# Kernel tuning notes

Hardware: AMD Instinct MI355X
Metric: run time of the kernel (lower is better)

Reference implementation:

```python
import jax, jax.numpy as jnp
import numpy as np
from jax.ops import segment_sum, segment_max

N_NODES, SEQ, D, V = 2048, 64, 256, 32000
NH, DH = 8, 32      # transformer heads, head dim
GH = 4              # GAT heads (concat=False -> mean over heads)
E = 32768
NEG_INF = -1e9


def _pe(max_len, d):
    pos = np.arange(max_len)[:, None].astype(np.float32)
    div = np.exp(np.arange(0, d, 2).astype(np.float32) * (-np.log(10000.0) / d))
    pe = np.zeros((max_len, d), np.float32)
    pe[:, 0::2] = np.sin(pos * div)
    pe[:, 1::2] = np.cos(pos * div)
    return jnp.asarray(pe)


def _ln(x, g, b, eps=1e-5):
    m = x.mean(-1, keepdims=True)
    v = jnp.var(x, axis=-1, keepdims=True)
    return (x - m) / jnp.sqrt(v + eps) * g + b


def _encoder(x, Wqkv, bqkv, Wo, bo, ln1g, ln1b, ln2g, ln2b, W1, b1, W2, b2):
    # nn.TransformerEncoder, post-norm, relu, dropout off (eval)
    for l in range(2):
        qkv = x @ Wqkv[l] + bqkv[l]
        q, k, v = jnp.split(qkv, 3, -1)
        hds = lambda t: t.reshape(N_NODES, SEQ, NH, DH).transpose(0, 2, 1, 3)
        q, k, v = hds(q), hds(k), hds(v)
        att = jax.nn.softmax(jnp.einsum('bhqd,bhkd->bhqk', q, k) / np.sqrt(DH).astype(np.float32), -1)
        o = jnp.einsum('bhqk,bhkd->bhqd', att, v).transpose(0, 2, 1, 3).reshape(N_NODES, SEQ, D)
        x = _ln(x + o @ Wo[l] + bo[l], ln1g[l], ln1b[l])
        ff = jax.nn.relu(x @ W1[l] + b1[l]) @ W2[l] + b2[l]
        x = _ln(x + ff, ln2g[l], ln2b[l])
    return x


def _gat(xt, W, b, asrc, adst, src, dst, emask):
    # PyG GATConv(heads=4, concat=False): self-loops added, LeakyReLU(0.2),
    # softmax over incoming edges per destination, mean over heads, + bias.
    x = (xt @ W).reshape(N_NODES, GH, D)              # [N,GH,D]
    a_s = jnp.sum(x * asrc, -1)                        # [N,GH]
    a_d = jnp.sum(x * adst, -1)
    e = jax.nn.leaky_relu(a_s[src] + a_d[dst], 0.2)    # [E,GH]
    e = jnp.where(emask[:, None], e, NEG_INF)
    e_self = jax.nn.leaky_relu(a_s + a_d, 0.2)         # [N,GH] self loops
    m = jnp.maximum(segment_max(e, dst, num_segments=N_NODES), e_self)
    w = jnp.where(emask[:, None], jnp.exp(e - m[dst]), 0.0)
    w_self = jnp.exp(e_self - m)
    denom = segment_sum(w, dst, num_segments=N_NODES) + w_self
    num = segment_sum(w[:, :, None] * x[src], dst, num_segments=N_NODES) + w_self[:, :, None] * x
    return (num / denom[:, :, None]).mean(1) + b


def setup_inputs():
    key = jax.random.key(0)
    ks = iter(jax.random.split(key, 40))
    g = lambda shape, s=0.02: jax.random.normal(next(ks), shape, jnp.float32) * s
    return dict(
        tok_emb=g((V, D)),
        enc_Wqkv=g((2, D, 3 * D)), enc_bqkv=jnp.zeros((2, 3 * D)),
        enc_Wo=g((2, D, D)), enc_bo=jnp.zeros((2, D)),
        enc_ln1_g=jnp.ones((2, D)), enc_ln1_b=jnp.zeros((2, D)),
        enc_ln2_g=jnp.ones((2, D)), enc_ln2_b=jnp.zeros((2, D)),
        enc_W1=g((2, D, D)), enc_b1=jnp.zeros((2, D)),
        enc_W2=g((2, D, D)), enc_b2=jnp.zeros((2, D)),
        type_emb=g((10, D)),
        msg_W=g((3, D, D)), msg_b=jnp.zeros((3, D)),
        gat_W=g((4, D, GH * D)), gat_b=jnp.zeros((4, D)),
        gat_asrc=g((4, GH, D)), gat_adst=g((4, GH, D)),
        sp_W1=g((D, 512)), sp_b1=jnp.zeros((512,)),
        sp_W2=g((512, D)), sp_b2=jnp.zeros((D,)),
        log_c=jnp.zeros((1,)),
        rule_token_seqs=jax.random.randint(next(ks), (N_NODES, SEQ), 0, V),
        rule_types=jax.random.randint(next(ks), (N_NODES,), 0, 10),
        edge_index=jax.random.randint(next(ks), (2, E), 0, N_NODES),
        edge_type=jax.random.randint(next(ks), (E,), 0, 3),
    )


def reference(tok_emb, enc_Wqkv, enc_bqkv, enc_Wo, enc_bo, enc_ln1_g, enc_ln1_b,
              enc_ln2_g, enc_ln2_b, enc_W1, enc_b1, enc_W2, enc_b2, type_emb,
              msg_W, msg_b, gat_W, gat_b, gat_asrc, gat_adst,
              sp_W1, sp_b1, sp_W2, sp_b2, log_c,
              rule_token_seqs, rule_types, edge_index, edge_type):
    # logic encoder
    x = tok_emb[rule_token_seqs] * np.sqrt(D).astype(np.float32) + _pe(SEQ, D)[None]
    x = _encoder(x, enc_Wqkv, enc_bqkv, enc_Wo, enc_bo, enc_ln1_g, enc_ln1_b,
                 enc_ln2_g, enc_ln2_b, enc_W1, enc_b1, enc_W2, enc_b2)
    h = x.mean(1) + type_emb[rule_types]                 # node_features [N,D]
    # logical GNN: per-relation linear + GATConv, summed, residual, relu
    src, dst = edge_index[0], edge_index[1]
    for l in range(4):
        h_new = 0.0
        for r in range(3):
            th = h @ msg_W[r] + msg_b[r]
            h_new = h_new + _gat(th, gat_W[l], gat_b[l], gat_asrc[l], gat_adst[l],
                                 src, dst, edge_type == r)
        h = jax.nn.relu(h + h_new)
    pos = jax.nn.relu(h @ sp_W1 + sp_b1) @ sp_W2 + sp_b2
    tang = jnp.tanh(pos) * 2.0
    st = tang * jnp.sqrt(jnp.exp(log_c))                 # scaled tangent [N,D]
    # Lorentz exp_map0 of v = [0, st]: ||v||_L = ||st||
    r = jnp.maximum(jnp.linalg.norm(st, axis=-1, keepdims=True), 1e-8)
    return jnp.concatenate([jnp.cosh(r), jnp.sinh(r) / r * st], -1)  # [N, D+1]
```

## Files before the change

kernel.cpp:

```cpp
#include <hip/hip_runtime.h>
#include <hip/hip_bf16.h>

#define NN 2048
#define SEQL 64
#define DIM 256
#define NHEAD 8
#define EDGES 32768
#define CHUNKS 2
#define CN (NN / CHUNKS)
#define CROWS (CN * SEQL)

typedef __attribute__((ext_vector_type(8))) short short8;
typedef __attribute__((ext_vector_type(4))) float f32x4;
typedef __attribute__((ext_vector_type(4))) unsigned short us4;
typedef unsigned short ushort_t;

__device__ __forceinline__ float us2f(unsigned short u) {
    union { unsigned int i; float f; } x; x.i = ((unsigned int)u) << 16; return x.f;
}
__device__ __forceinline__ unsigned short f2us(float f) {
    union { float f; unsigned int i; } u; u.f = f;
    unsigned int r = u.i + 0x7fffu + ((u.i >> 16) & 1u);
    return (unsigned short)(r >> 16);
}
__device__ __forceinline__ float lrelu02(float v) { return v < 0.f ? 0.2f * v : v; }

__device__ __forceinline__ void gload_lds16(const void* g, void* l) {
    __builtin_amdgcn_global_load_lds(
        (const __attribute__((address_space(1))) unsigned int*)g,
        (__attribute__((address_space(3))) unsigned int*)l, 16, 0, 0);
}

__global__ void sniff_kernel(const unsigned int* __restrict__ w, int* __restrict__ flag) {
    __shared__ int cnt;
    if (threadIdx.x == 0) cnt = 0;
    __syncthreads();
    unsigned int v = w[(size_t)threadIdx.x * 509];
    unsigned int e_lo = (v >> 7) & 0xffu;
    if (e_lo >= 0x6eu && e_lo <= 0x7fu) atomicAdd(&cnt, 1);
    __syncthreads();
    if (threadIdx.x == 0) *flag = (cnt > 128) ? 1 : 0;
}

#define NE 33
struct ConvArgs {
    const void* src[NE];
    unsigned int soff[NE];
    unsigned int off[NE + 1];
    unsigned int nel[NE];
    unsigned short ncol[NE];
    unsigned char klog2[NE];
};

__global__ void convert_kernel(ConvArgs a, const int* __restrict__ flag,
                               ushort_t* __restrict__ dst, unsigned int total) {
    const int bf = *flag;
    for (unsigned int i = blockIdx.x * 256 + threadIdx.x; i < total; i += gridDim.x * 256) {
        int e = 0;
        while (a.off[e + 1] <= i) ++e;
        unsigned int j = i - a.off[e];
        ushort_t v = 0;
        if (j < a.nel[e]) {
            unsigned int sidx;
            if (a.klog2[e]) {
                unsigned int K = 1u << a.klog2[e];
                unsigned int k = j & (K - 1), n = j >> a.klog2[e];
                sidx = k * (unsigned int)a.ncol[e] + n;
            } else sidx = j;
            sidx += a.soff[e];
            if (bf) v = ((const ushort_t*)a.src[e])[sidx];
            else    v = f2us(((const float*)a.src[e])[sidx]);
        }
        dst[i] = v;
    }
}

template <bool RELU, bool OUT_BF16>
__global__ __launch_bounds__(256) void gemm_bt(
    const ushort_t* __restrict__ A, const ushort_t* __restrict__ BT,
    const ushort_t* __restrict__ bias, void* __restrict__ C,
    int M, int N, int K, int lda, size_t a_off_z, size_t c_off_z)
{
    __shared__ __align__(16) short a_lds[2][128][32];
    __shared__ __align__(16) short b_lds[2][128][32];

    const int tid  = threadIdx.x;
    const int lane = tid & 63;
    const int wave = tid >> 6;
    const int wr = wave >> 1, wc = wave & 1;
    const size_t mbase = (size_t)blockIdx.x * 128;
    const size_t nbase = (size_t)blockIdx.y * 128;
    A += (size_t)blockIdx.z * a_off_z;
    const size_t czoff = (size_t)blockIdx.z * c_off_z;

    f32x4 acc[4][4];
    const f32x4 fzero = {0.f, 0.f, 0.f, 0.f};
#pragma unroll
    for (int i = 0; i < 4; ++i)
#pragma unroll
        for (int j = 0; j < 4; ++j) acc[i][j] = fzero;

    const int srow = tid >> 2;
    const int ksw0 = (((tid & 3) ^ ((srow >> 1) & 3)) * 8);
    const int rl = lane & 15;
    const int kfs = (((lane >> 4) ^ ((rl >> 1) & 3)) * 8);

    const int nk = K >> 5;
    auto stage = [&](int buf, int k0) {
        short* lA = &a_lds[buf][0][0] + wave * 512;
        short* lB = &b_lds[buf][0][0] + wave * 512;
        gload_lds16(A  + (mbase + srow)      * (size_t)lda + k0 + ksw0, lA);
        gload_lds16(A  + (mbase + srow + 64) * (size_t)lda + k0 + ksw0, lA + 2048);
        gload_lds16(BT + (nbase + srow)      * (size_t)K   + k0 + ksw0, lB);
        gload_lds16(BT + (nbase + srow + 64) * (size_t)K   + k0 + ksw0, lB + 2048);
    };

    stage(0, 0);
    __syncthreads();
    for (int t = 0; t < nk; ++t) {
        const int cur = t & 1;
        if (t + 1 < nk) stage(cur ^ 1, (t + 1) * 32);

        short8 af[4], bfr[4];
#pragma unroll
        for (int m = 0; m < 4; ++m) af[m]  = *(const short8*)&a_lds[cur][wr * 64 + m * 16 + rl][kfs];
#pragma unroll
        for (int n = 0; n < 4; ++n) bfr[n] = *(const short8*)&b_lds[cur][wc * 64 + n * 16 + rl][kfs];
#pragma unroll
        for (int m = 0; m < 4; ++m)
#pragma unroll
            for (int n = 0; n < 4; ++n)
                acc[m][n] = __builtin_amdgcn_mfma_f32_16x16x32_bf16(af[m], bfr[n], acc[m][n], 0, 0, 0);
        if (t + 1 < nk) __syncthreads();
    }

    const int rq = (lane >> 4) * 4;
#pragma unroll
    for (int m = 0; m < 4; ++m) {
#pragma unroll
        for (int n = 0; n < 4; ++n) {
            size_t gcol = nbase + wc * 64 + n * 16 + rl;
            float bv = bias ? us2f(bias[gcol]) : 0.f;
#pragma unroll
            for (int q = 0; q < 4; ++q) {
                size_t grow = mbase + wr * 64 + m * 16 + rq + q;
                float v = acc[m][n][q] + bv;
                if (RELU) v = fmaxf(v, 0.f);
                if (OUT_BF16) ((ushort_t*)C)[czoff + grow * N + gcol] = f2us(v);
                else          ((float*)C)[czoff + grow * N + gcol] = v;
            }
        }
    }
}

__global__ __launch_bounds__(512) void gemm_ln(
    const ushort_t* __restrict__ A, const ushort_t* __restrict__ BT,
    const ushort_t* __restrict__ bias, ushort_t* __restrict__ X,
    const ushort_t* __restrict__ gg, const ushort_t* __restrict__ bb, int K)
{
    __shared__ __align__(16) short a_lds[2][128][32];
    __shared__ __align__(16) short b_lds[2][256][32];
    __shared__ float st_part[128][8];
    __shared__ float st_fin[128][2];

    const int tid  = threadIdx.x;
    const int lane = tid & 63;
    const int wave = tid >> 6;
    const int wr = wave >> 2, wc = wave & 3;
    const size_t mbase = (size_t)blockIdx.x * 128;

    f32x4 acc[4][4];
    const f32x4 fzero = {0.f, 0.f, 0.f, 0.f};
#pragma unroll
    for (int i = 0; i < 4; ++i)
#pragma unroll
        for (int j = 0; j < 4; ++j) acc[i][j] = fzero;

    const int srow = tid >> 2;
    const int ksw0 = (((tid & 3) ^ ((srow >> 1) & 3)) * 8);
    const int rl = lane & 15;
    const int g  = lane >> 4;
    const int kfs = ((g ^ ((rl >> 1) & 3)) * 8);

    const int nk = K >> 5;
    auto stage = [&](int buf, int k0) {
        gload_lds16(A  + (mbase + srow) * (size_t)K + k0 + ksw0,
                    &a_lds[buf][0][0] + wave * 512);
        gload_lds16(BT + (size_t)srow         * K + k0 + ksw0,
                    &b_lds[buf][0][0] + wave * 512);
        gload_lds16(BT + (size_t)(srow + 128) * K + k0 + ksw0,
                    &b_lds[buf][0][0] + wave * 512 + 4096);
    };

    stage(0, 0);
    __syncthreads();
    for (int t = 0; t < nk; ++t) {
        const int cur = t & 1;
        if (t + 1 < nk) stage(cur ^ 1, (t + 1) * 32);

        short8 af[4], bfr[4];
#pragma unroll
        for (int m = 0; m < 4; ++m) af[m]  = *(const short8*)&a_lds[cur][wr * 64 + m * 16 + rl][kfs];
#pragma unroll
        for (int n = 0; n < 4; ++n) bfr[n] = *(const short8*)&b_lds[cur][wc * 64 + n * 16 + rl][kfs];
#pragma unroll
        for (int m = 0; m < 4; ++m)
#pragma unroll
            for (int n = 0; n < 4; ++n)
                acc[m][n] = __builtin_amdgcn_mfma_f32_16x16x32_bf16(af[m], bfr[n], acc[m][n], 0, 0, 0);
        if (t + 1 < nk) __syncthreads();
    }

#pragma unroll
    for (int m = 0; m < 4; ++m)
#pragma unroll
        for (int n = 0; n < 4; ++n) {
            int gcol = wc * 64 + n * 16 + rl;
            float bv = us2f(bias[gcol]);
#pragma unroll
            for (int r = 0; r < 4; ++r) {
                size_t grow = mbase + wr * 64 + m * 16 + g * 4 + r;
                acc[m][n][r] += bv + us2f(X[grow * 256 + gcol]);
            }
        }
#pragma unroll
    for (int m = 0; m < 4; ++m)
#pragma unroll
        for (int r = 0; r < 4; ++r) {
            float ps = 0.f, pq = 0.f;
#pragma unroll
            for (int n = 0; n < 4; ++n) { float v = acc[m][n][r]; ps += v; pq += v * v; }
#pragma unroll
            for (int off = 1; off < 16; off <<= 1) { ps += __shfl_xor(ps, off); pq += __shfl_xor(pq, off); }
            if (rl == 0) {
                int row = wr * 64 + m * 16 + g * 4 + r;
                st_part[row][wc] = ps;
                st_part[row][4 + wc] = pq;
            }
        }
    __syncthreads();
    if (tid < 128) {
        float s = st_part[tid][0] + st_part[tid][1] + st_part[tid][2] + st_part[tid][3];
        float q = st_part[tid][4] + st_part[tid][5] + st_part[tid][6] + st_part[tid][7];
        float mean = s * (1.f / 256.f);
        float var = q * (1.f / 256.f) - mean * mean;
        st_fin[tid][0] = mean;
        st_fin[tid][1] = rsqrtf(var + 1e-5f);
    }
    __syncthreads();
#pragma unroll
    for (int m = 0; m < 4; ++m)
#pragma unroll
        for (int n = 0; n < 4; ++n) {
            int gcol = wc * 64 + n * 16 + rl;
            float gv = us2f(gg[gcol]), bv = us2f(bb[gcol]);
#pragma unroll
            for (int r = 0; r < 4; ++r) {
                int row = wr * 64 + m * 16 + g * 4 + r;
                float out = (acc[m][n][r] - st_fin[row][0]) * st_fin[row][1] * gv + bv;
                X[(mbase + row) * 256 + gcol] = f2us(out);
            }
        }
}

__global__ __launch_bounds__(128) void attn_mfma(const ushort_t* __restrict__ qkv,
                                                 ushort_t* __restrict__ O) {
    __shared__ ushort_t smem[2][6912];
    const int w = threadIdx.x >> 6, lane = threadIdx.x & 63;
    const int h = blockIdx.y * 2 + w;
    const int rl = lane & 15, g = lane >> 4;
    const size_t rowbase = (size_t)blockIdx.x * 64;
    ushort_t* vt = smem[w];
    ushort_t* pl = smem[w] + 2304;

    const ushort_t* vp = qkv + (rowbase + lane) * 768 + 512 + h * 32;
#pragma unroll
    for (int i = 0; i < 4; ++i) {
        union { short8 v; ushort_t s[8]; } u;
        u.v = *(const short8*)(vp + i * 8);
#pragma unroll
        for (int j = 0; j < 8; ++j) vt[(i * 8 + j) * 72 + lane] = u.s[j];
    }

    short8 kf[4], qf[4];
#pragma unroll
    for (int t = 0; t < 4; ++t) {
        kf[t] = *(const short8*)(qkv + (rowbase + t * 16 + rl) * 768 + 256 + h * 32 + g * 8);
        qf[t] = *(const short8*)(qkv + (rowbase + t * 16 + rl) * 768 +       h * 32 + g * 8);
    }

    f32x4 s[4][4];
    const f32x4 fzero = {0.f, 0.f, 0.f, 0.f};
#pragma unroll
    for (int kt = 0; kt < 4; ++kt)
#pragma unroll
        for (int qt = 0; qt < 4; ++qt) s[kt][qt] = fzero;
#pragma unroll
    for (int kt = 0; kt < 4; ++kt)
#pragma unroll
        for (int qt = 0; qt < 4; ++qt)
            s[kt][qt] = __builtin_amdgcn_mfma_f32_16x16x32_bf16(kf[kt], qf[qt], s[kt][qt], 0, 0, 0);

    const float sc = 0.17677669529663687f;
    float inv[4];
#pragma unroll
    for (int qt = 0; qt < 4; ++qt) {
        float m = -1e30f;
#pragma unroll
        for (int kt = 0; kt < 4; ++kt)
#pragma unroll
            for (int r = 0; r < 4; ++r) { s[kt][qt][r] *= sc; m = fmaxf(m, s[kt][qt][r]); }
        m = fmaxf(m, __shfl_xor(m, 16));
        m = fmaxf(m, __shfl_xor(m, 32));
        float sum = 0.f;
#pragma unroll
        for (int kt = 0; kt < 4; ++kt)
#pragma unroll
            for (int r = 0; r < 4; ++r) { float e = __expf(s[kt][qt][r] - m); s[kt][qt][r] = e; sum += e; }
        sum += __shfl_xor(sum, 16);
        sum += __shfl_xor(sum, 32);
        inv[qt] = 1.f / sum;
    }

#pragma unroll
    for (int qt = 0; qt < 4; ++qt)
#pragma unroll
        for (int kt = 0; kt < 4; ++kt) {
            us4 pk;
#pragma unroll
            for (int r = 0; r < 4; ++r) pk[r] = f2us(s[kt][qt][r] * inv[qt]);
            *(us4*)&pl[(qt * 16 + rl) * 72 + kt * 16 + g * 4] = pk;
        }
    asm volatile("s_waitcnt lgkmcnt(0)" ::: "memory");
    __builtin_amdgcn_sched_barrier(0);

    f32x4 o[2][4];
#pragma unroll
    for (int dt = 0; dt < 2; ++dt)
#pragma unroll
        for (int qt = 0; qt < 4; ++qt) o[dt][qt] = fzero;
#pragma unroll
    for (int ks = 0; ks < 2; ++ks) {
        short8 va[2];
#pragma unroll
        for (int dt = 0; dt < 2; ++dt)
            va[dt] = *(const short8*)&vt[(dt * 16 + rl) * 72 + ks * 32 + g * 8];
#pragma unroll
        for (int qt = 0; qt < 4; ++qt) {
            short8 pb = *(const short8*)&pl[(qt * 16 + rl) * 72 + ks * 32 + g * 8];
#pragma unroll
            for (int dt = 0; dt < 2; ++dt)
                o[dt][qt] = __builtin_amdgcn_mfma_f32_16x16x32_bf16(va[dt], pb, o[dt][qt], 0, 0, 0);
        }
    }

#pragma unroll
    for (int dt = 0; dt < 2; ++dt)
#pragma unroll
        for (int qt = 0; qt < 4; ++qt) {
            us4 ov;
#pragma unroll
            for (int r = 0; r < 4; ++r) ov[r] = f2us(o[dt][qt][r]);
            *(us4*)&pl[(qt * 16 + rl) * 40 + dt * 16 + g * 4] = ov;
        }
    asm volatile("s_waitcnt lgkmcnt(0)" ::: "memory");
    __builtin_amdgcn_sched_barrier(0);
    ushort_t* op = O + (rowbase + lane) * 256 + h * 32;
#pragma unroll
    for (int t = 0; t < 4; ++t)
        *(short8*)(op + t * 8) = *(const short8*)&pl[lane * 40 + t * 8];
}

__global__ void pe_kernel(float* __restrict__ pe) {
    int s = blockIdx.x, d = threadIdx.x;
    int i = d >> 1;
    float freq = __expf((float)(2 * i) * (-9.210340371976184f / 256.f));
    float ang = (float)s * freq;
    pe[s * DIM + d] = (d & 1) ? cosf(ang) : sinf(ang);
}

__global__ __launch_bounds__(64) void embed_kernel(const void* __restrict__ tok_emb,
                                                   const int* __restrict__ flag,
                                                   const int* __restrict__ tokens,
                                                   const float* __restrict__ pe,
                                                   ushort_t* __restrict__ X, int row0) {
    int lr = blockIdx.x, t = threadIdx.x;
    int grow = row0 + lr;
    int tok = tokens[grow];
    int s = grow & 63;
    int d0 = t * 4;
    size_t idx = (size_t)tok * DIM + d0;
    f32x4 pv = *(const f32x4*)&pe[s * DIM + d0];
    us4 out;
    if (*flag) {
        us4 tv = *(const us4*)((const ushort_t*)tok_emb + idx);
#pragma unroll
        for (int j = 0; j < 4; ++j) out[j] = f2us(us2f(tv[j]) * 16.f + pv[j]);
    } else {
        f32x4 tv = *(const f32x4*)((const float*)tok_emb + idx);
#pragma unroll
        for (int j = 0; j < 4; ++j) out[j] = f2us(tv[j] * 16.f + pv[j]);
    }
    *(us4*)&X[(size_t)lr * DIM + d0] = out;
}

__global__ void mean_kernel(const ushort_t* __restrict__ Xc,
                            const ushort_t* __restrict__ type_emb,
                            const int* __restrict__ rtypes,
                            float* __restrict__ h, ushort_t* __restrict__ hb, int n0) {
    int nl = blockIdx.x, d = threadIdx.x;
    float acc = 0.f;
    for (int s = 0; s < 64; ++s) acc += us2f(Xc[((size_t)nl * 64 + s) * DIM + d]);
    int n = n0 + nl;
    float val = acc * (1.f / 64.f) + us2f(type_emb[(size_t)rtypes[n] * DIM + d]);
    h[(size_t)n * DIM + d] = val;
    hb[(size_t)n * DIM + d] = f2us(val);
}

__global__ void hist_kernel(const int* __restrict__ ei, int* __restrict__ counts) {
    int e = blockIdx.x * 256 + threadIdx.x;
    if (e < EDGES) atomicAdd(&counts[ei[EDGES + e]], 1);
}
__global__ __launch_bounds__(256) void scan_kernel(const int* __restrict__ counts,
                                                   int* __restrict__ indptr,
                                                   int* __restrict__ cursor) {
    __shared__ int part[256];
    int t = threadIdx.x;
    int local[8]; int s = 0;
#pragma unroll
    for (int i = 0; i < 8; ++i) { local[i] = s; s += counts[t * 8 + i]; }
    part[t] = s;
    __syncthreads();
    for (int d = 1; d < 256; d <<= 1) {
        int val = (t >= d) ? part[t - d] : 0;
        __syncthreads();
        part[t] += val;
        __syncthreads();
    }
    int base = part[t] - s;
#pragma unroll
    for (int i = 0; i < 8; ++i) { int v = base + local[i]; indptr[t * 8 + i] = v; cursor[t * 8 + i] = v; }
    if (t == 255) indptr[NN] = part[255];
}
__global__ void scatter_kernel(const int* __restrict__ ei, const int* __restrict__ et,
                               int* __restrict__ cursor, int* __restrict__ col_src,
                               int* __restrict__ col_type) {
    int e = blockIdx.x * 256 + threadIdx.x;
    if (e < EDGES) {
        int d = ei[EDGES + e];
        int pp = atomicAdd(&cursor[d], 1);
        col_src[pp] = ei[e];
        col_type[pp] = et[e];
    }
}

__global__ __launch_bounds__(256) void asad_kernel(const float* __restrict__ xg,
                                                   const ushort_t* __restrict__ asrc,
                                                   const ushort_t* __restrict__ adst,
                                                   float* __restrict__ a_s, float* __restrict__ a_d,
                                                   int l) {
    int n = blockIdx.x, r = blockIdx.y, g = threadIdx.x >> 6, lane = threadIdx.x & 63;
    const float* xp = xg + ((size_t)r * NN + n) * 1024 + g * 256 + lane * 4;
    const ushort_t* sp = asrc + ((size_t)l * 4 + g) * 256 + lane * 4;
    const ushort_t* dp = adst + ((size_t)l * 4 + g) * 256 + lane * 4;
    float ss = 0.f, dd = 0.f;
#pragma unroll
    for (int j = 0; j < 4; ++j) { float x = xp[j]; ss += x * us2f(sp[j]); dd += x * us2f(dp[j]); }
#pragma unroll
    for (int off = 32; off > 0; off >>= 1) { ss += __shfl_xor(ss, off); dd += __shfl_xor(dd, off); }
    if (lane == 0) {
        a_s[((size_t)r * NN + n) * 4 + g] = ss;
        a_d[((size_t)r * NN + n) * 4 + g] = dd;
    }
}

__global__ __launch_bounds__(256) void edge_kernel(const float* __restrict__ xg,
                                                   const float* __restrict__ a_s,
                                                   const float* __restrict__ a_d,
                                                   const int* __restrict__ indptr,
                                                   const int* __restrict__ col_src,
                                                   const int* __restrict__ col_type,
                                                   const ushort_t* __restrict__ gat_b,
                                                   float* __restrict__ hnew3, int l) {
    __shared__ float outs[4][256];
    int n = blockIdx.x, r = blockIdx.y, g = threadIdx.x >> 6, lane = threadIdx.x & 63;
    int beg = indptr[n], end = indptr[n + 1];
    const size_t rb = (size_t)r * NN;
    float adn = a_d[(rb + n) * 4 + g];
    float eself = lrelu02(a_s[(rb + n) * 4 + g] + adn);
    float m = eself;
    for (int e = beg; e < end; ++e) {
        if (col_type[e] == r) {
            float v = lrelu02(a_s[(rb + col_src[e]) * 4 + g] + adn);
            m = fmaxf(m, v);
        }
    }
    float wself = __expf(eself - m);
    float denom = wself;
    const float* xn = xg + (rb + n) * 1024 + g * 256 + lane * 4;
    float num[4];
#pragma unroll
    for (int j = 0; j < 4; ++j) num[j] = wself * xn[j];
    for (int e = beg; e < end; ++e) {
        if (col_type[e] == r) {
            int src = col_src[e];
            float v = lrelu02(a_s[(rb + src) * 4 + g] + adn);
            float w = __expf(v - m);
            denom += w;
            const float* xs = xg + (rb + src) * 1024 + g * 256 + lane * 4;
#pragma unroll
            for (int j = 0; j < 4; ++j) num[j] += w * xs[j];
        }
    }
    float invd = 1.f / denom;
#pragma unroll
    for (int j = 0; j < 4; ++j) outs[g][lane * 4 + j] = num[j] * invd;
    __syncthreads();
    int d = threadIdx.x;
    float hv = 0.25f * (outs[0][d] + outs[1][d] + outs[2][d] + outs[3][d]) + us2f(gat_b[l * 256 + d]);
    hnew3[(rb + n) * 256 + d] = hv;
}

__global__ void update_h_kernel(float* __restrict__ h, const float* __restrict__ hnew3,
                                ushort_t* __restrict__ hb) {
    size_t i = (size_t)blockIdx.x * 256 + threadIdx.x;
    float v = fmaxf(h[i] + hnew3[i] + hnew3[(size_t)NN * 256 + i] + hnew3[(size_t)2 * NN * 256 + i], 0.f);
    h[i] = v;
    hb[i] = f2us(v);
}

__global__ __launch_bounds__(64) void final_kernel(const float* __restrict__ pos,
                                                   const ushort_t* __restrict__ log_c,
                                                   const int* __restrict__ flag,
                                                   void* __restrict__ out) {
    int n = blockIdx.x, lane = threadIdx.x;
    int bf = *flag;
    float scv = sqrtf(__expf(us2f(log_c[0])));
    f32x4 pv = *(const f32x4*)&pos[(size_t)n * 256 + lane * 4];
    float st[4]; float sq = 0.f;
#pragma unroll
    for (int j = 0; j < 4; ++j) { float t = tanhf(pv[j]) * 2.f * scv; st[j] = t; sq += t * t; }
#pragma unroll
    for (int off = 32; off > 0; off >>= 1) sq += __shfl_xor(sq, off);
    float rr = fmaxf(sqrtf(sq), 1e-8f);
    float sf = sinhf(rr) / rr;
    if (bf) {
        ushort_t* o = (ushort_t*)out;
        if (lane == 0) o[(size_t)n * 257] = f2us(coshf(rr));
#pragma unroll
        for (int j = 0; j < 4; ++j) o[(size_t)n * 257 + 1 + lane * 4 + j] = f2us(sf * st[j]);
    } else {
        float* o = (float*)out;
        if (lane == 0) o[(size_t)n * 257] = coshf(rr);
#pragma unroll
        for (int j = 0; j < 4; ++j) o[(size_t)n * 257 + 1 + lane * 4 + j] = sf * st[j];
    }
}

extern "C" void kernel_launch(void* const* d_in, const int* in_sizes, int n_in,
                              void* d_out, int out_size, void* d_ws, size_t ws_size,
                              hipStream_t stream) {
    const int* tokens = (const int*)d_in[25];
    const int* rtypes = (const int*)d_in[26];
    const int* eidx   = (const int*)d_in[27];
    const int* etype  = (const int*)d_in[28];

    char* base = (char*)d_ws;
    size_t pos = 0;
    auto alloc = [&](size_t b) -> char* {
        char* r = base + pos; pos = (pos + b + 255) & ~(size_t)255; return r;
    };

    int* flag = (int*)alloc(256);

    ConvArgs ca;
    int ne = 0; unsigned int off = 0;
    auto add = [&](const void* src, unsigned int soff, unsigned int elems,
                   int klog2, int ncol) -> unsigned int {
        ca.src[ne] = src; ca.soff[ne] = soff; ca.off[ne] = off;
        ca.nel[ne] = elems; ca.klog2[ne] = (unsigned char)klog2;
        ca.ncol[ne] = (unsigned short)ncol;
        unsigned int r = off; off += (elems + 7) & ~7u; ++ne; return r;
    };
    unsigned int oWqkv = add(d_in[1], 0, 196608, 8, 768);
                         add(d_in[1], 196608, 196608, 8, 768);
    unsigned int obqkv = add(d_in[2], 0, 1536, 0, 0);
    unsigned int oWo   = add(d_in[3], 0, 65536, 8, 256);
                         add(d_in[3], 65536, 65536, 8, 256);
    unsigned int obo   = add(d_in[4], 0, 512, 0, 0);
    unsigned int oln1g = add(d_in[5], 0, 512, 0, 0);
    unsigned int oln1b = add(d_in[6], 0, 512, 0, 0);
    unsigned int oln2g = add(d_in[7], 0, 512, 0, 0);
    unsigned int oln2b = add(d_in[8], 0, 512, 0, 0);
    unsigned int oW1   = add(d_in[9], 0, 65536, 8, 256);
                         add(d_in[9], 65536, 65536, 8, 256);
    unsigned int ob1   = add(d_in[10], 0, 512, 0, 0);
    unsigned int oW2   = add(d_in[11], 0, 65536, 8, 256);
                         add(d_in[11], 65536, 65536, 8, 256);
    unsigned int ob2   = add(d_in[12], 0, 512, 0, 0);
    unsigned int otype = add(d_in[13], 0, 2560, 0, 0);
    unsigned int omsgW = add(d_in[14], 0, 65536, 8, 256);
                         add(d_in[14], 65536, 65536, 8, 256);
                         add(d_in[14], 131072, 65536, 8, 256);
    unsigned int omsgb = add(d_in[15], 0, 768, 0, 0);
    unsigned int ogatW = add(d_in[16], 0, 262144, 8, 1024);
                         add(d_in[16], 262144, 262144, 8, 1024);
                         add(d_in[16], 524288, 262144, 8, 1024);
                         add(d_in[16], 786432, 262144, 8, 1024);
    unsigned int ogatb = add(d_in[17], 0, 1024, 0, 0);
    unsigned int oasrc = add(d_in[18], 0, 4096, 0, 0);
    unsigned int oadst = add(d_in[19], 0, 4096, 0, 0);
    unsigned int ospW1 = add(d_in[20], 0, 131072, 8, 512);
    unsigned int ospb1 = add(d_in[21], 0, 512, 0, 0);
    unsigned int ospW2 = add(d_in[22], 0, 131072, 9, 256);
    unsigned int ospb2 = add(d_in[23], 0, 256, 0, 0);
    unsigned int ologc = add(d_in[24], 0, 1, 0, 0);
    ca.off[ne] = off;
    unsigned int wtotal = off;

    ushort_t* wtb   = (ushort_t*)alloc((size_t)wtotal * 2);
    float*    pe    = (float*)   alloc((size_t)SEQL * DIM * 4);
    float*    h     = (float*)   alloc((size_t)NN * DIM * 4);
    ushort_t* hb    = (ushort_t*)alloc((size_t)NN * DIM * 2);
    float*    a_s   = (float*)   alloc((size_t)3 * NN * 4 * 4);
    float*    a_d   = (float*)   alloc((size_t)3 * NN * 4 * 4);
    int*      counts = (int*)    alloc((size_t)NN * 4);
    int*      indptr = (int*)    alloc((size_t)(NN + 1) * 4);
    int*      cursor = (int*)    alloc((size_t)NN * 4);
    int*      col_src  = (int*)  alloc((size_t)EDGES * 4);
    int*      col_type = (int*)  alloc((size_t)EDGES * 4);

    size_t spos0 = pos;
    ushort_t* Xc  = (ushort_t*)alloc((size_t)CROWS * DIM * 2);
    ushort_t* QKV = (ushort_t*)alloc((size_t)CROWS * 768 * 2);
    ushort_t* Oc  = (ushort_t*)alloc((size_t)CROWS * DIM * 2);
    pos = spos0;
    ushort_t* th    = (ushort_t*)alloc((size_t)NN * 768 * 2);
    float*    xg    = (float*)   alloc((size_t)3 * NN * 1024 * 4);
    float*    hnew3 = (float*)   alloc((size_t)3 * NN * DIM * 4);
    ushort_t* thead = (ushort_t*)alloc((size_t)NN * 512 * 2);
    float*    posb  = (float*)   alloc((size_t)NN * DIM * 4);

    const ushort_t* WqkvT = wtb + oWqkv;
    const ushort_t* bqkv  = wtb + obqkv;
    const ushort_t* WoT   = wtb + oWo;
    const ushort_t* bo    = wtb + obo;
    const ushort_t* ln1g  = wtb + oln1g;
    const ushort_t* ln1b  = wtb + oln1b;
    const ushort_t* ln2g  = wtb + oln2g;
    const ushort_t* ln2b  = wtb + oln2b;
    const ushort_t* W1T   = wtb + oW1;
    const ushort_t* b1    = wtb + ob1;
    const ushort_t* W2T   = wtb + oW2;
    const ushort_t* b2    = wtb + ob2;
    const ushort_t* type_emb = wtb + otype;
    const ushort_t* msgWT = wtb + omsgW;
    const ushort_t* msg_b = wtb + omsgb;
    const ushort_t* gatWT = wtb + ogatW;
    const ushort_t* gat_b = wtb + ogatb;
    const ushort_t* gasrc = wtb + oasrc;
    const ushort_t* gadst = wtb + oadst;
    const ushort_t* spW1T = wtb + ospW1;
    const ushort_t* spb1  = wtb + ospb1;
    const ushort_t* spW2T = wtb + ospW2;
    const ushort_t* spb2  = wtb + ospb2;
    const ushort_t* log_c = wtb + ologc;

    sniff_kernel<<<1, 256, 0, stream>>>((const unsigned int*)d_in[1], flag);
    convert_kernel<<<2048, 256, 0, stream>>>(ca, flag, wtb, wtotal);

    pe_kernel<<<SEQL, DIM, 0, stream>>>(pe);
    hipMemsetAsync(counts, 0, NN * 4, stream);
    hist_kernel<<<EDGES / 256, 256, 0, stream>>>(eidx, counts);
    scan_kernel<<<1, 256, 0, stream>>>(counts, indptr, cursor);
    scatter_kernel<<<EDGES / 256, 256, 0, stream>>>(eidx, etype, cursor, col_src, col_type);

    for (int c = 0; c < CHUNKS; ++c) {
        int row0 = c * CROWS;
        embed_kernel<<<CROWS, 64, 0, stream>>>(d_in[0], flag, tokens, pe, Xc, row0);
        for (int l = 0; l < 2; ++l) {
            gemm_bt<false, true><<<dim3(CROWS / 128, 6), 256, 0, stream>>>(
                Xc, WqkvT + (size_t)l * 196608, bqkv + l * 768, QKV, CROWS, 768, DIM, DIM, 0, 0);
            attn_mfma<<<dim3(CN, 4), 128, 0, stream>>>(QKV, Oc);
            gemm_ln<<<CROWS / 128, 512, 0, stream>>>(
                Oc, WoT + (size_t)l * 65536, bo + l * DIM, Xc, ln1g + l * DIM, ln1b + l * DIM, DIM);
            gemm_bt<true, true><<<dim3(CROWS / 128, 2), 256, 0, stream>>>(
                Xc, W1T + (size_t)l * 65536, b1 + l * DIM, Oc, CROWS, DIM, DIM, DIM, 0, 0);
            gemm_ln<<<CROWS / 128, 512, 0, stream>>>(
                Oc, W2T + (size_t)l * 65536, b2 + l * DIM, Xc, ln2g + l * DIM, ln2b + l * DIM, DIM);
        }
        mean_kernel<<<CN, DIM, 0, stream>>>(Xc, type_emb, rtypes, h, hb, c * CN);
    }

    for (int l = 0; l < 4; ++l) {
        gemm_bt<false, true><<<dim3(NN / 128, 6), 256, 0, stream>>>(
            hb, msgWT, msg_b, th, NN, 768, DIM, DIM, 0, 0);
        gemm_bt<false, false><<<dim3(NN / 128, 8, 3), 256, 0, stream>>>(
            th, gatWT + (size_t)l * 262144, nullptr, xg, NN, 1024, DIM, 768,
            (size_t)256, (size_t)NN * 1024);
        asad_kernel<<<dim3(NN, 3), 256, 0, stream>>>(xg, gasrc, gadst, a_s, a_d, l);
        edge_kernel<<<dim3(NN, 3), 256, 0, stream>>>(xg, a_s, a_d, indptr, col_src, col_type,
                                                     gat_b, hnew3, l);
        update_h_kernel<<<NN, 256, 0, stream>>>(h, hnew3, hb);
    }

    gemm_bt<true, true><<<dim3(NN / 128, 4), 256, 0, stream>>>(
        hb, spW1T, spb1, thead, NN, 512, DIM, DIM, 0, 0);
    gemm_bt<false, false><<<dim3(NN / 128, 2), 256, 0, stream>>>(
        thead, spW2T, spb2, posb, NN, DIM, 512, 512, 0, 0);
    final_kernel<<<NN, 64, 0, stream>>>(posb, log_c, flag, d_out);
}
```

Measured before the change: 1.192 ms.

## Pipeline GEMM k-loop two stages deep with manual waitcnt and XCD-aware block remap

```diff
diff --git a/kernel.cpp b/kernel.cpp
--- a/kernel.cpp
+++ b/kernel.cpp
@@ -75,11 +75,11 @@
     }
 }
 
-template <bool RELU, bool OUT_BF16>
+template <int K, bool RELU, bool OUT_BF16>
 __global__ __launch_bounds__(256) void gemm_bt(
     const ushort_t* __restrict__ A, const ushort_t* __restrict__ BT,
     const ushort_t* __restrict__ bias, void* __restrict__ C,
-    int M, int N, int K, int lda, size_t a_off_z, size_t c_off_z)
+    int N, int lda, size_t a_off_z, size_t c_off_z)
 {
     __shared__ __align__(16) short a_lds[2][128][32];
     __shared__ __align__(16) short b_lds[2][128][32];
@@ -88,8 +88,17 @@
     const int lane = tid & 63;
     const int wave = tid >> 6;
     const int wr = wave >> 1, wc = wave & 1;
-    const size_t mbase = (size_t)blockIdx.x * 128;
-    const size_t nbase = (size_t)blockIdx.y * 128;
+
+    const int gx = gridDim.x, gy = gridDim.y;
+    const int nwg = gx * gy;
+    const int lin = blockIdx.y * gx + blockIdx.x;
+    const int q8 = nwg >> 3;
+    const int sid = (lin & 7) * q8 + (lin >> 3);
+    const int mb = sid / gy;
+    const int nb = sid - mb * gy;
+    const size_t mbase = (size_t)mb * 128;
+    const size_t nbase = (size_t)nb * 128;
+
     A += (size_t)blockIdx.z * a_off_z;
     const size_t czoff = (size_t)blockIdx.z * c_off_z;
 
@@ -105,7 +114,7 @@
     const int rl = lane & 15;
     const int kfs = (((lane >> 4) ^ ((rl >> 1) & 3)) * 8);
 
-    const int nk = K >> 5;
+    constexpr int nk = K >> 5;
     auto stage = [&](int buf, int k0) {
         short* lA = &a_lds[buf][0][0] + wave * 512;
         short* lB = &b_lds[buf][0][0] + wave * 512;
@@ -116,22 +125,30 @@
     };
 
     stage(0, 0);
-    __syncthreads();
+    if (nk > 1) stage(1, 32);
+#pragma unroll
     for (int t = 0; t < nk; ++t) {
         const int cur = t & 1;
-        if (t + 1 < nk) stage(cur ^ 1, (t + 1) * 32);
+        if (t + 1 < nk) { asm volatile("s_waitcnt vmcnt(4)" ::: "memory"); }
+        else            { asm volatile("s_waitcnt vmcnt(0)" ::: "memory"); }
+        __builtin_amdgcn_s_barrier();
+        __builtin_amdgcn_sched_barrier(0);
 
         short8 af[4], bfr[4];
 #pragma unroll
         for (int m = 0; m < 4; ++m) af[m]  = *(const short8*)&a_lds[cur][wr * 64 + m * 16 + rl][kfs];
 #pragma unroll
         for (int n = 0; n < 4; ++n) bfr[n] = *(const short8*)&b_lds[cur][wc * 64 + n * 16 + rl][kfs];
+        asm volatile("s_waitcnt lgkmcnt(0)" ::: "memory");
+        __builtin_amdgcn_sched_barrier(0);
 #pragma unroll
         for (int m = 0; m < 4; ++m)
 #pragma unroll
             for (int n = 0; n < 4; ++n)
                 acc[m][n] = __builtin_amdgcn_mfma_f32_16x16x32_bf16(af[m], bfr[n], acc[m][n], 0, 0, 0);
-        if (t + 1 < nk) __syncthreads();
+        __builtin_amdgcn_s_barrier();
+        __builtin_amdgcn_sched_barrier(0);
+        if (t + 2 < nk) stage(cur, (t + 2) * 32);
     }
 
     const int rq = (lane >> 4) * 4;
@@ -142,9 +159,9 @@
             size_t gcol = nbase + wc * 64 + n * 16 + rl;
             float bv = bias ? us2f(bias[gcol]) : 0.f;
 #pragma unroll
-            for (int q = 0; q < 4; ++q) {
-                size_t grow = mbase + wr * 64 + m * 16 + rq + q;
-                float v = acc[m][n][q] + bv;
+            for (int p = 0; p < 4; ++p) {
+                size_t grow = mbase + wr * 64 + m * 16 + rq + p;
+                float v = acc[m][n][p] + bv;
                 if (RELU) v = fmaxf(v, 0.f);
                 if (OUT_BF16) ((ushort_t*)C)[czoff + grow * N + gcol] = f2us(v);
                 else          ((float*)C)[czoff + grow * N + gcol] = v;
@@ -153,10 +170,11 @@
     }
 }
 
+template <int K>
 __global__ __launch_bounds__(512) void gemm_ln(
     const ushort_t* __restrict__ A, const ushort_t* __restrict__ BT,
     const ushort_t* __restrict__ bias, ushort_t* __restrict__ X,
-    const ushort_t* __restrict__ gg, const ushort_t* __restrict__ bb, int K)
+    const ushort_t* __restrict__ gg, const ushort_t* __restrict__ bb)
 {
     __shared__ __align__(16) short a_lds[2][128][32];
     __shared__ __align__(16) short b_lds[2][256][32];
@@ -182,7 +200,7 @@
     const int g  = lane >> 4;
     const int kfs = ((g ^ ((rl >> 1) & 3)) * 8);
 
-    const int nk = K >> 5;
+    constexpr int nk = K >> 5;
     auto stage = [&](int buf, int k0) {
         gload_lds16(A  + (mbase + srow) * (size_t)K + k0 + ksw0,
                     &a_lds[buf][0][0] + wave * 512);
@@ -193,22 +211,30 @@
     };
 
     stage(0, 0);
-    __syncthreads();
+    if (nk > 1) stage(1, 32);
+#pragma unroll
     for (int t = 0; t < nk; ++t) {
         const int cur = t & 1;
-        if (t + 1 < nk) stage(cur ^ 1, (t + 1) * 32);
+        if (t + 1 < nk) { asm volatile("s_waitcnt vmcnt(3)" ::: "memory"); }
+        else            { asm volatile("s_waitcnt vmcnt(0)" ::: "memory"); }
+        __builtin_amdgcn_s_barrier();
+        __builtin_amdgcn_sched_barrier(0);
 
         short8 af[4], bfr[4];
 #pragma unroll
         for (int m = 0; m < 4; ++m) af[m]  = *(const short8*)&a_lds[cur][wr * 64 + m * 16 + rl][kfs];
 #pragma unroll
         for (int n = 0; n < 4; ++n) bfr[n] = *(const short8*)&b_lds[cur][wc * 64 + n * 16 + rl][kfs];
+        asm volatile("s_waitcnt lgkmcnt(0)" ::: "memory");
+        __builtin_amdgcn_sched_barrier(0);
 #pragma unroll
         for (int m = 0; m < 4; ++m)
 #pragma unroll
             for (int n = 0; n < 4; ++n)
                 acc[m][n] = __builtin_amdgcn_mfma_f32_16x16x32_bf16(af[m], bfr[n], acc[m][n], 0, 0, 0);
-        if (t + 1 < nk) __syncthreads();
+        __builtin_amdgcn_s_barrier();
+        __builtin_amdgcn_sched_barrier(0);
+        if (t + 2 < nk) stage(cur, (t + 2) * 32);
     }
 
 #pragma unroll
@@ -679,24 +705,24 @@
         int row0 = c * CROWS;
         embed_kernel<<<CROWS, 64, 0, stream>>>(d_in[0], flag, tokens, pe, Xc, row0);
         for (int l = 0; l < 2; ++l) {
-            gemm_bt<false, true><<<dim3(CROWS / 128, 6), 256, 0, stream>>>(
-                Xc, WqkvT + (size_t)l * 196608, bqkv + l * 768, QKV, CROWS, 768, DIM, DIM, 0, 0);
+            gemm_bt<256, false, true><<<dim3(CROWS / 128, 6), 256, 0, stream>>>(
+                Xc, WqkvT + (size_t)l * 196608, bqkv + l * 768, QKV, 768, DIM, 0, 0);
             attn_mfma<<<dim3(CN, 4), 128, 0, stream>>>(QKV, Oc);
-            gemm_ln<<<CROWS / 128, 512, 0, stream>>>(
-                Oc, WoT + (size_t)l * 65536, bo + l * DIM, Xc, ln1g + l * DIM, ln1b + l * DIM, DIM);
-            gemm_bt<true, true><<<dim3(CROWS / 128, 2), 256, 0, stream>>>(
-                Xc, W1T + (size_t)l * 65536, b1 + l * DIM, Oc, CROWS, DIM, DIM, DIM, 0, 0);
-            gemm_ln<<<CROWS / 128, 512, 0, stream>>>(
-                Oc, W2T + (size_t)l * 65536, b2 + l * DIM, Xc, ln2g + l * DIM, ln2b + l * DIM, DIM);
+            gemm_ln<256><<<CROWS / 128, 512, 0, stream>>>(
+                Oc, WoT + (size_t)l * 65536, bo + l * DIM, Xc, ln1g + l * DIM, ln1b + l * DIM);
+            gemm_bt<256, true, true><<<dim3(CROWS / 128, 2), 256, 0, stream>>>(
+                Xc, W1T + (size_t)l * 65536, b1 + l * DIM, Oc, DIM, DIM, 0, 0);
+            gemm_ln<256><<<CROWS / 128, 512, 0, stream>>>(
+                Oc, W2T + (size_t)l * 65536, b2 + l * DIM, Xc, ln2g + l * DIM, ln2b + l * DIM);
         }
         mean_kernel<<<CN, DIM, 0, stream>>>(Xc, type_emb, rtypes, h, hb, c * CN);
     }
 
     for (int l = 0; l < 4; ++l) {
-        gemm_bt<false, true><<<dim3(NN / 128, 6), 256, 0, stream>>>(
-            hb, msgWT, msg_b, th, NN, 768, DIM, DIM, 0, 0);
-        gemm_bt<false, false><<<dim3(NN / 128, 8, 3), 256, 0, stream>>>(
-            th, gatWT + (size_t)l * 262144, nullptr, xg, NN, 1024, DIM, 768,
+        gemm_bt<256, false, true><<<dim3(NN / 128, 6), 256, 0, stream>>>(
+            hb, msgWT, msg_b, th, 768, DIM, 0, 0);
+        gemm_bt<256, false, false><<<dim3(NN / 128, 8, 3), 256, 0, stream>>>(
+            th, gatWT + (size_t)l * 262144, nullptr, xg, 1024, 768,
             (size_t)256, (size_t)NN * 1024);
         asad_kernel<<<dim3(NN, 3), 256, 0, stream>>>(xg, gasrc, gadst, a_s, a_d, l);
         edge_kernel<<<dim3(NN, 3), 256, 0, stream>>>(xg, a_s, a_d, indptr, col_src, col_type,
@@ -704,9 +730,9 @@
         update_h_kernel<<<NN, 256, 0, stream>>>(h, hnew3, hb);
     }
 
-    gemm_bt<true, true><<<dim3(NN / 128, 4), 256, 0, stream>>>(
-        hb, spW1T, spb1, thead, NN, 512, DIM, DIM, 0, 0);
-    gemm_bt<false, false><<<dim3(NN / 128, 2), 256, 0, stream>>>(
-        thead, spW2T, spb2, posb, NN, DIM, 512, 512, 0, 0);
+    gemm_bt<256, true, true><<<dim3(NN / 128, 4), 256, 0, stream>>>(
+        hb, spW1T, spb1, thead, 512, DIM, 0, 0);
+    gemm_bt<512, false, false><<<dim3(NN / 128, 2), 256, 0, stream>>>(
+        thead, spW2T, spb2, posb, DIM, 512, 0, 0);
     final_kernel<<<NN, 64, 0, stream>>>(posb, log_c, flag, d_out);
 }
```

After: 1.126 ms. 1.06x faster.
